# Performance work log

Hardware: AMD Instinct MI355X
Metric: run time of the kernel (lower is better)

Reference implementation:

```python
import jax, jax.numpy as jnp
import numpy as np

N_STARS = 2048   # n_stars
BATCH = 256      # query positions per call
PF = 28          # poly_features = (d_max+1)(d_max+2)/2, d_max=6
NGE = 512        # n_graph_elems
GF = 32          # graph_features
OPD = 256        # opd_dim


def setup_inputs() -> dict:
    key = jax.random.key(0)
    ks = jax.random.split(key, 8)
    # observed star positions in the FoV (x_lims/y_lims = [0,1000])
    obs_pos = jax.random.uniform(ks[0], (N_STARS, 2), jnp.float32, 0.0, 1000.0)
    # query positions are exact rows of obs_pos (required by the exact-match index search)
    idx = jax.random.randint(ks[1], (BATCH,), 0, N_STARS)
    positions = obs_pos[idx]
    poly_dic = jax.random.normal(ks[2], (N_STARS, PF), jnp.float32)
    graph_dic = jax.random.normal(ks[3], (N_STARS, NGE), jnp.float32)
    # alpha matrices: identity(-padded) init as in init_vars, plus small noise
    alpha_poly = jnp.eye(PF, dtype=jnp.float32) + 0.01 * jax.random.normal(ks[4], (PF, PF), jnp.float32)
    alpha_graph = (jnp.eye(NGE, GF, dtype=jnp.float32)
                   + 0.01 * jax.random.normal(ks[5], (NGE, GF), jnp.float32))
    # S features: random uniform in [-1e-3, 1e-3] as in init_vars
    S_poly = jax.random.uniform(ks[6], (PF, OPD, OPD), jnp.float32, -0.001, 0.001)
    S_graph = jax.random.uniform(ks[7], (GF, OPD, OPD), jnp.float32, -0.001, 0.001)
    return {
        'positions': positions, 'obs_pos': obs_pos,
        'poly_dic': poly_dic, 'graph_dic': graph_dic,
        'alpha_poly': alpha_poly, 'alpha_graph': alpha_graph,
        'S_poly': S_poly, 'S_graph': S_graph,
    }


def _calc_indices(positions, obs_pos):
    # Faithful to tf.where(tf.equal(obs_pos, pos))[0, 0]: first True entry (row-major)
    # of the elementwise equality over (n_stars, 2); its row index is taken.
    eq = positions[:, None, :] == obs_pos[None, :, :]          # (B, N, 2) bool
    flat_first = jnp.argmax(eq.reshape(eq.shape[0], -1), axis=1)  # first True, flat index
    return flat_first // 2                                      # row index in obs_pos


def reference(positions, obs_pos, poly_dic, graph_dic, alpha_poly, alpha_graph, S_poly, S_graph):
    indices = _calc_indices(positions, obs_pos)                 # (B,) int
    # polynomial part: gather -> matmul -> tensordot with OPD modes
    batch_poly = jnp.take(poly_dic, indices, axis=0)            # (B, PF)
    interm_poly = batch_poly @ alpha_poly                       # (B, PF)
    contrib_poly = jnp.einsum('bp,pij->bij', interm_poly, S_poly)  # (B, OPD, OPD)
    # graph part
    batch_graph = jnp.take(graph_dic, indices, axis=0)          # (B, NGE)
    interm_graph = batch_graph @ alpha_graph                    # (B, GF)
    contrib_graph = jnp.einsum('bg,gij->bij', interm_graph, S_graph)
    return contrib_poly + contrib_graph
```

## Files before the change

kernel.cpp:

```cpp
#include <hip/hip_runtime.h>

#define NSTARS 2048
#define BATCH  256
#define PF     28
#define NGE    512
#define GF     32
#define OPD2   65536
#define KTOT   (PF + GF)
#define TM     32

__global__ __launch_bounds__(256) void prep_kernel(
    const float* __restrict__ positions,  const float* __restrict__ obs_pos,
    const float* __restrict__ poly_dic,   const float* __restrict__ graph_dic,
    const float* __restrict__ alpha_poly, const float* __restrict__ alpha_graph,
    float* __restrict__ Wt)
{
    const int b = blockIdx.x;
    const int t = threadIdx.x;

    const float p0 = positions[2 * b];
    const float p1 = positions[2 * b + 1];

    int cand = 0x7fffffff;
    #pragma unroll
    for (int i = 0; i < NSTARS / 256; ++i) {
        const int n = t + i * 256;
        const float o0 = obs_pos[2 * n];
        const float o1 = obs_pos[2 * n + 1];
        if (o0 == p0 || o1 == p1) cand = min(cand, n);
    }
    __shared__ int smin[256];
    smin[t] = cand;
    __syncthreads();
    for (int s = 128; s > 0; s >>= 1) {
        if (t < s) smin[t] = min(smin[t], smin[t + s]);
        __syncthreads();
    }
    int idx = smin[0];
    if (idx == 0x7fffffff) idx = 0;

    if (t < PF) {
        float acc = 0.f;
        #pragma unroll
        for (int p = 0; p < PF; ++p)
            acc += poly_dic[idx * PF + p] * alpha_poly[p * PF + t];
        Wt[t * BATCH + b] = acc;
    }

    __shared__ float psum[8][GF];
    {
        const int g = t & 31;
        const int r = t >> 5;
        float acc = 0.f;
        const int e0 = r * (NGE / 8);
        for (int e = e0; e < e0 + NGE / 8; ++e)
            acc += graph_dic[idx * NGE + e] * alpha_graph[e * GF + g];
        psum[r][g] = acc;
    }
    __syncthreads();
    if (t < GF) {
        float acc = 0.f;
        #pragma unroll
        for (int r = 0; r < 8; ++r) acc += psum[r][t];
        Wt[(PF + t) * BATCH + b] = acc;
    }
}

__global__ __launch_bounds__(256) void main_kernel(
    const float* __restrict__ S_poly, const float* __restrict__ S_graph,
    const float* __restrict__ Wt, float* __restrict__ out)
{
    const int t  = threadIdx.x;
    const int ij = blockIdx.x * 1024 + t * 4;
    const int b0 = blockIdx.y * TM;

    float4 acc[TM];
    #pragma unroll
    for (int b = 0; b < TM; ++b) acc[b] = make_float4(0.f, 0.f, 0.f, 0.f);

    const float* __restrict__ wp = Wt + b0;

    #pragma unroll 2
    for (int k = 0; k < PF; ++k) {
        const float4 s = *reinterpret_cast<const float4*>(
            S_poly + (size_t)k * OPD2 + ij);
        #pragma unroll
        for (int b = 0; b < TM; ++b) {
            const float w = wp[k * BATCH + b];
            acc[b].x += w * s.x;
            acc[b].y += w * s.y;
            acc[b].z += w * s.z;
            acc[b].w += w * s.w;
        }
    }
    #pragma unroll 2
    for (int k = 0; k < GF; ++k) {
        const float4 s = *reinterpret_cast<const float4*>(
            S_graph + (size_t)k * OPD2 + ij);
        #pragma unroll
        for (int b = 0; b < TM; ++b) {
            const float w = wp[(PF + k) * BATCH + b];
            acc[b].x += w * s.x;
            acc[b].y += w * s.y;
            acc[b].z += w * s.z;
            acc[b].w += w * s.w;
        }
    }

    #pragma unroll
    for (int b = 0; b < TM; ++b) {
        *reinterpret_cast<float4*>(out + (size_t)(b0 + b) * OPD2 + ij) = acc[b];
    }
}

extern "C" void kernel_launch(void* const* d_in, const int* in_sizes, int n_in,
                              void* d_out, int out_size, void* d_ws, size_t ws_size,
                              hipStream_t stream) {
    const float* positions   = (const float*)d_in[0];
    const float* obs_pos     = (const float*)d_in[1];
    const float* poly_dic    = (const float*)d_in[2];
    const float* graph_dic   = (const float*)d_in[3];
    const float* alpha_poly  = (const float*)d_in[4];
    const float* alpha_graph = (const float*)d_in[5];
    const float* S_poly      = (const float*)d_in[6];
    const float* S_graph     = (const float*)d_in[7];
    float* out = (float*)d_out;

    float* Wt = (float*)d_ws;

    prep_kernel<<<BATCH, 256, 0, stream>>>(positions, obs_pos, poly_dic,
                                           graph_dic, alpha_poly, alpha_graph,
                                           Wt);

    dim3 grid(OPD2 / 1024, BATCH / TM);
    main_kernel<<<grid, 256, 0, stream>>>(S_poly, S_graph, Wt, out);
}
```

Baseline: 126.7 us.

## Keep S column in registers and stream batch groups with nontemporal stores

```diff
diff --git a/kernel.cpp b/kernel.cpp
--- a/kernel.cpp
+++ b/kernel.cpp
@@ -7,7 +7,8 @@
 #define GF     32
 #define OPD2   65536
 #define KTOT   (PF + GF)
-#define TM     32
+
+typedef float v8f __attribute__((ext_vector_type(8)));
 
 __global__ __launch_bounds__(256) void prep_kernel(
     const float* __restrict__ positions,  const float* __restrict__ obs_pos,
@@ -66,50 +67,33 @@
     }
 }
 
-__global__ __launch_bounds__(256) void main_kernel(
+__global__ __launch_bounds__(256, 4) void main_kernel(
     const float* __restrict__ S_poly, const float* __restrict__ S_graph,
     const float* __restrict__ Wt, float* __restrict__ out)
 {
     const int t  = threadIdx.x;
-    const int ij = blockIdx.x * 1024 + t * 4;
-    const int b0 = blockIdx.y * TM;
+    const int ij = blockIdx.x * 256 + t;
+    const int bq = blockIdx.y * 64;
 
-    float4 acc[TM];
+    float s[KTOT];
     #pragma unroll
-    for (int b = 0; b < TM; ++b) acc[b] = make_float4(0.f, 0.f, 0.f, 0.f);
+    for (int k = 0; k < PF; ++k) s[k]      = S_poly[(size_t)k * OPD2 + ij];
+    #pragma unroll
+    for (int k = 0; k < GF; ++k) s[PF + k] = S_graph[(size_t)k * OPD2 + ij];
 
-    const float* __restrict__ wp = Wt + b0;
-
-    #pragma unroll 2
-    for (int k = 0; k < PF; ++k) {
-        const float4 s = *reinterpret_cast<const float4*>(
-            S_poly + (size_t)k * OPD2 + ij);
+    for (int g = 0; g < 8; ++g) {
+        const int b0 = bq + g * 8;
+        float acc[8] = {0.f, 0.f, 0.f, 0.f, 0.f, 0.f, 0.f, 0.f};
         #pragma unroll
-        for (int b = 0; b < TM; ++b) {
-            const float w = wp[k * BATCH + b];
-            acc[b].x += w * s.x;
-            acc[b].y += w * s.y;
-            acc[b].z += w * s.z;
-            acc[b].w += w * s.w;
+        for (int k = 0; k < KTOT; ++k) {
+            const v8f w = *reinterpret_cast<const v8f*>(Wt + k * BATCH + b0);
+            #pragma unroll
+            for (int j = 0; j < 8; ++j) acc[j] += s[k] * w[j];
         }
-    }
-    #pragma unroll 2
-    for (int k = 0; k < GF; ++k) {
-        const float4 s = *reinterpret_cast<const float4*>(
-            S_graph + (size_t)k * OPD2 + ij);
         #pragma unroll
-        for (int b = 0; b < TM; ++b) {
-            const float w = wp[(PF + k) * BATCH + b];
-            acc[b].x += w * s.x;
-            acc[b].y += w * s.y;
-            acc[b].z += w * s.z;
-            acc[b].w += w * s.w;
-        }
-    }
-
-    #pragma unroll
-    for (int b = 0; b < TM; ++b) {
-        *reinterpret_cast<float4*>(out + (size_t)(b0 + b) * OPD2 + ij) = acc[b];
+        for (int j = 0; j < 8; ++j)
+            __builtin_nontemporal_store(acc[j],
+                out + (size_t)(b0 + j) * OPD2 + ij);
     }
 }
 
@@ -132,6 +116,6 @@
                                            graph_dic, alpha_poly, alpha_graph,
                                            Wt);
 
-    dim3 grid(OPD2 / 1024, BATCH / TM);
+    dim3 grid(OPD2 / 256, 4);
     main_kernel<<<grid, 256, 0, stream>>>(S_poly, S_graph, Wt, out);
 }
```

New measurement: 142.1 us. 1.12x slower.
